# Performance work log

Measured on AMD Instinct MI355X. Metric: run time of the kernel, lower is better.

## Reference

```python
import jax, jax.numpy as jnp
import numpy as np
from jax import lax

VOCAB = 50257; IN_DIM = 1024; MEM = 1024
ATT_UNITS = 256; HOPS = 16
H1 = 1024; H2 = 512; H3 = 256; CLASSES = 5
N = 512  # maxlen == number of tree nodes (pad() is a no-op, penalty mask is zero)


def _build_tree(n):
    # Binary heap tree relabeled to DFS post-order ranks, so children always
    # have smaller rank than their parent and H accumulates in the same order
    # as the original recursive torch code.
    order = []
    def post(j):
        for c in (2 * j + 1, 2 * j + 2):
            if c < n:
                post(c)
        order.append(j)
    post(0)
    rank = {j: r for r, j in enumerate(order)}
    child_idx = np.zeros((n, 2), np.int32)
    mask = np.zeros((n, 2), np.float32)
    for j in range(n):
        r = rank[j]
        for k, c in enumerate((2 * j + 1, 2 * j + 2)):
            if c < n:
                child_idx[r, k] = rank[c]
                mask[r, k] = 1.0
    return jnp.asarray(child_idx), jnp.asarray(mask)


def setup_inputs() -> dict:
    key = jax.random.key(0)
    ks = jax.random.split(key, 24)
    def w(k, shape, s=0.05):
        return jax.random.normal(k, shape, jnp.float32) * s
    child_idx, child_mask = _build_tree(N)
    return {
        "linputs": jax.random.randint(ks[0], (N,), 0, VOCAB, jnp.int32),
        "rinputs": jax.random.randint(ks[1], (N,), 0, VOCAB, jnp.int32),
        "child_idx": child_idx,
        "child_mask": child_mask,
        "emb": w(ks[2], (VOCAB, IN_DIM)),
        "w_ioux": w(ks[3], (3 * MEM, IN_DIM)), "b_ioux": w(ks[4], (3 * MEM,)),
        "w_iouh": w(ks[5], (3 * MEM, MEM)), "b_iouh": w(ks[6], (3 * MEM,)),
        "w_fx": w(ks[7], (MEM, IN_DIM)), "b_fx": w(ks[8], (MEM,)),
        "w_fh": w(ks[9], (MEM, MEM)), "b_fh": w(ks[10], (MEM,)),
        "ws1": w(ks[11], (ATT_UNITS, MEM)),
        "ws2": w(ks[12], (HOPS, ATT_UNITS)),
        "wf": w(ks[13], (1, MEM, H1)),
        "w_lat": w(ks[14], (1, HOPS)), "b_lat": w(ks[15], (1,)),
        "w_fc": w(ks[16], (H2, 3 * H1)), "b_fc": w(ks[17], (H2,)),
        "w_out": w(ks[18], (H3, H2)), "b_out": w(ks[19], (H3,)),
        "w_out1": w(ks[20], (CLASSES, H3)), "b_out1": w(ks[21], (CLASSES,)),
    }


def _tree_lstm(x, child_idx, child_mask, w_ioux, b_ioux, w_iouh, b_iouh,
               w_fx, b_fx, w_fh, b_fh):
    # x: [N, in_dim]; nodes in post-order (children before parent).
    # Leaf case of the original (single all-zero child) is reproduced exactly
    # by masked (zero) child rows: child_h_sum = 0 and sum(f * child_c) = 0.
    n = x.shape[0]
    mem = w_fh.shape[0]
    x_iou = x @ w_ioux.T + b_ioux  # [N, 3M], precomputed input projections
    x_f = x @ w_fx.T + b_fx        # [N, M]

    def step(carry, xs):
        C, Hs = carry
        i, ci, m, xiou, xf = xs
        ch = Hs[ci] * m[:, None]   # [2, M] masked child hidden states
        cc = C[ci] * m[:, None]    # [2, M] masked child cell states
        iou = xiou + ch.sum(0) @ w_iouh.T + b_iouh
        ig, og, ug = jnp.split(iou, 3)
        ig = jax.nn.sigmoid(ig); og = jax.nn.sigmoid(og); ug = jnp.tanh(ug)
        f = jax.nn.sigmoid(ch @ w_fh.T + b_fh + xf)  # [2, M] forget per child
        c = ig * ug + (f * cc).sum(0)
        h = og * jnp.tanh(c)
        return (C.at[i].set(c), Hs.at[i].set(h)), None

    z = jnp.zeros((n, mem), x.dtype)
    (C, Hs), _ = lax.scan(step, (z, z),
                          (jnp.arange(n), child_idx, child_mask, x_iou, x_f))
    return Hs  # H stacked in DFS post-order; root hidden is Hs[-1]


def _attend(H, ws1, ws2):
    # H: [N, M]; N == maxlen so the penalty term of the original is all-zero.
    hbar = jnp.tanh(H @ ws1.T)                           # [N, att_units]
    alphas = jax.nn.softmax((hbar @ ws2.T).T, axis=-1)   # [hops, N]
    return alphas @ H, alphas[None]                      # [hops, M], [1, hops, N]


def reference(linputs, rinputs, child_idx, child_mask, emb,
              w_ioux, b_ioux, w_iouh, b_iouh, w_fx, b_fx, w_fh, b_fh,
              ws1, ws2, wf, w_lat, b_lat, w_fc, b_fc, w_out, b_out,
              w_out1, b_out1):
    tl = lambda tok: _tree_lstm(emb[tok], child_idx, child_mask,
                                w_ioux, b_ioux, w_iouh, b_iouh,
                                w_fx, b_fx, w_fh, b_fh)
    Hl = tl(linputs)
    Hr = tl(rinputs)
    Ml, attl = _attend(Hl, ws1, ws2)
    Mr, attr = _attend(Hr, ws1, ws2)
    lstate = jax.nn.relu(Ml @ wf[0])   # [hops, H1]
    rstate = jax.nn.relu(Mr @ wf[0])
    # lat_att applied on transposed matrix == left-multiply by its weight row
    lvec = w_lat @ lstate + b_lat      # [1, H1]
    rvec = w_lat @ rstate + b_lat
    fr = jnp.concatenate([jnp.abs(lvec - rvec), lvec * rvec,
                          0.5 * (lvec + rvec)], axis=1)  # [1, 3*H1]
    fc = jax.nn.leaky_relu(fr @ w_fc.T + b_fc, 0.01)
    fc2 = jax.nn.sigmoid(fc @ w_out.T + b_out)
    out = jax.nn.log_softmax(fc2 @ w_out1.T + b_out1, axis=-1)  # [1, classes]
    return out, attl, attr
```

## Files before the change

kernel.cpp:

```cpp
#include <hip/hip_runtime.h>
#include <math.h>

#define NN 512
#define MEMD 1024

typedef __attribute__((ext_vector_type(8))) short short8;
typedef __attribute__((ext_vector_type(4))) float float4v;

struct Sched {
  int child0[NN]; int child1[NN];
  float m0[NN]; float m1[NN];
  int chrow[2 * NN];
  int order[NN];
  int lvl_off[12];
};

constexpr void post_order_rec(int j, int n, int (&ord)[NN], int& cnt) {
  if (2 * j + 1 < n) post_order_rec(2 * j + 1, n, ord, cnt);
  if (2 * j + 2 < n) post_order_rec(2 * j + 2, n, ord, cnt);
  ord[cnt++] = j;
}

constexpr Sched make_sched() {
  Sched s{};
  int ord[NN] = {}; int cnt = 0;
  post_order_rec(0, NN, ord, cnt);
  int rank[NN] = {};
  for (int r = 0; r < NN; ++r) rank[ord[r]] = r;
  for (int j = 0; j < NN; ++j) {
    int r = rank[j];
    int c0 = 2 * j + 1, c1 = 2 * j + 2;
    s.child0[r] = (c0 < NN) ? rank[c0] : 0;
    s.m0[r] = (c0 < NN) ? 1.0f : 0.0f;
    s.child1[r] = (c1 < NN) ? rank[c1] : 0;
    s.m1[r] = (c1 < NN) ? 1.0f : 0.0f;
  }
  int h[NN] = {};
  for (int r = 0; r < NN; ++r) {
    int hh = 0;
    if (s.m0[r] > 0.0f) { int t = h[s.child0[r]] + 1; if (t > hh) hh = t; }
    if (s.m1[r] > 0.0f) { int t = h[s.child1[r]] + 1; if (t > hh) hh = t; }
    h[r] = hh;
  }
  int counts[12] = {};
  for (int r = 0; r < NN; ++r) counts[h[r]]++;
  s.lvl_off[0] = 0;
  for (int l = 0; l < 11; ++l) s.lvl_off[l + 1] = s.lvl_off[l] + counts[l];
  int pos[12] = {};
  for (int l = 0; l < 12; ++l) pos[l] = s.lvl_off[l];
  for (int r = 0; r < NN; ++r) s.order[pos[h[r]]++] = r;
  for (int slot = 0; slot < NN; ++slot) {
    int r = s.order[slot];
    s.chrow[2 * slot + 0] = (s.m0[r] > 0.f) ? s.child0[r] : -1;
    s.chrow[2 * slot + 1] = (s.m1[r] > 0.f) ? s.child1[r] : -1;
  }
  return s;
}

static constexpr Sched g_sched = make_sched();
__constant__ Sched c_sched = g_sched;

__device__ __forceinline__ float sigm(float x) { return 1.0f / (1.0f + expf(-x)); }

__device__ __forceinline__ unsigned short f2bf(float f) {
  union { float f; unsigned int u; } v; v.f = f;
  unsigned int r = v.u + 0x7fffu + ((v.u >> 16) & 1u);
  return (unsigned short)(r >> 16);
}

__device__ __forceinline__ void glds16(const unsigned short* g, unsigned short* l) {
  __builtin_amdgcn_global_load_lds(
      (const __attribute__((address_space(1))) void*)g,
      (__attribute__((address_space(3))) void*)l, 16, 0, 0);
}

__global__ __launch_bounds__(256) void k_cast_w(
    const float* __restrict__ w_ioux, const float* __restrict__ w_fx,
    const float* __restrict__ w_iouh, const float* __restrict__ w_fh,
    const float* __restrict__ ws1,
    unsigned short* __restrict__ Wx, unsigned short* __restrict__ Wh,
    unsigned short* __restrict__ Ws1b)
{
  const int b = (int)blockIdx.x;
  const float* src; unsigned short* dst;
  if (b < 4096) {
    dst = Wx + (size_t)b * 1024;
    src = (b < 3072) ? w_ioux + (size_t)b * 1024 : w_fx + (size_t)(b - 3072) * 1024;
  } else if (b < 8192) {
    int r = b - 4096;
    dst = Wh + (size_t)r * 1024;
    src = (r < 3072) ? w_iouh + (size_t)r * 1024 : w_fh + (size_t)(r - 3072) * 1024;
  } else {
    int r = b - 8192;
    dst = Ws1b + (size_t)r * 1024;
    src = ws1 + (size_t)r * 1024;
  }
  const int t4 = threadIdx.x * 4;
  float4 v = *(const float4*)(src + t4);
  ushort4 o;
  o.x = f2bf(v.x); o.y = f2bf(v.y); o.z = f2bf(v.z); o.w = f2bf(v.w);
  *(ushort4*)(dst + t4) = o;
}

__global__ __launch_bounds__(256) void k_cast_emb(
    const int* __restrict__ lin, const int* __restrict__ rin,
    const float* __restrict__ emb, unsigned short* __restrict__ Ae,
    unsigned short* __restrict__ Hb)
{
  const int r = (int)blockIdx.x;
  if (r == 1024) {
    ushort4 z; z.x = 0; z.y = 0; z.z = 0; z.w = 0;
    *(ushort4*)(Hb + (size_t)1024 * 1024 + threadIdx.x * 4) = z;
    return;
  }
  const int tok = (r < 512) ? lin[r] : rin[r - 512];
  const float* src = emb + (size_t)tok * 1024;
  const int t4 = threadIdx.x * 4;
  float4 v = *(const float4*)(src + t4);
  ushort4 o;
  o.x = f2bf(v.x); o.y = f2bf(v.y); o.z = f2bf(v.z); o.w = f2bf(v.w);
  *(ushort4*)(Ae + (size_t)r * 1024 + t4) = o;
}

__global__ __launch_bounds__(256) void k_gemm(
    const unsigned short* __restrict__ A, const unsigned short* __restrict__ B,
    float* __restrict__ Cout, int M, int N, int off, int R)
{
  __shared__ unsigned short As[2][128 * 64];
  __shared__ unsigned short Bs[2][128 * 64];
  const int tid = threadIdx.x;
  const int L = tid & 63, w = tid >> 6;
  const int bx = (int)blockIdx.x, by = (int)blockIdx.y;
  const int z = (int)blockIdx.z;
  const int nt = 16 / (int)gridDim.z;
  const int k0 = z * nt * 64;
  const int q = (L & 7) ^ (L >> 3);

  const unsigned short* ga[4];
  const unsigned short* gb[4];
  #pragma unroll
  for (int i = 0; i < 4; ++i) {
    int c = w * 4 + i;
    int r = 8 * c + (L >> 3);
    int u = bx * 128 + r;
    int arow;
    if (off < 0) {
      arow = u;
    } else {
      if (u >= 4 * R) arow = 1024;
      else {
        int t = (u >= 2 * R) ? 1 : 0;
        int rr = u - t * 2 * R;
        int ch = c_sched.chrow[2 * (off + (rr >> 1)) + (rr & 1)];
        arow = (ch < 0) ? 1024 : t * 512 + ch;
      }
    }
    ga[i] = A + (size_t)arow * 1024 + k0 + q * 8;
    gb[i] = B + (size_t)(by * 128 + r) * 1024 + k0 + q * 8;
  }

  float4v acc[4][4];
  #pragma unroll
  for (int i = 0; i < 4; ++i)
    #pragma unroll
    for (int j = 0; j < 4; ++j) acc[i][j] = (float4v)(0.0f);

  const int wm = (w & 1) * 64, wn = (w >> 1) * 64;
  const int lr = L & 15, lq = L >> 4;

  #pragma unroll
  for (int i = 0; i < 4; ++i) {
    glds16(ga[i], &As[0][(w * 4 + i) * 512]);
    glds16(gb[i], &Bs[0][(w * 4 + i) * 512]);
    ga[i] += 64; gb[i] += 64;
  }
  __syncthreads();

  int cur = 0;
  for (int kk = 0; kk < nt; ++kk) {
    if (kk + 1 < nt) {
      #pragma unroll
      for (int i = 0; i < 4; ++i) {
        glds16(ga[i], &As[cur ^ 1][(w * 4 + i) * 512]);
        glds16(gb[i], &Bs[cur ^ 1][(w * 4 + i) * 512]);
        ga[i] += 64; gb[i] += 64;
      }
    }
    const unsigned short* Ac = &As[cur][0];
    const unsigned short* Bc = &Bs[cur][0];
    #pragma unroll
    for (int kh = 0; kh < 2; ++kh) {
      short8 af[4], bf[4];
      #pragma unroll
      for (int mi = 0; mi < 4; ++mi) {
        int tr = wm + mi * 16 + lr;
        af[mi] = *(const short8*)(Ac + tr * 64 + (((kh * 4 + lq) ^ (tr & 7)) * 8));
      }
      #pragma unroll
      for (int ni = 0; ni < 4; ++ni) {
        int tr = wn + ni * 16 + lr;
        bf[ni] = *(const short8*)(Bc + tr * 64 + (((kh * 4 + lq) ^ (tr & 7)) * 8));
      }
      #pragma unroll
      for (int mi = 0; mi < 4; ++mi)
        #pragma unroll
        for (int ni = 0; ni < 4; ++ni)
          acc[mi][ni] = __builtin_amdgcn_mfma_f32_16x16x32_bf16(
              af[mi], bf[ni], acc[mi][ni], 0, 0, 0);
    }
    __syncthreads();
    cur ^= 1;
  }

  float* Cz = Cout + (size_t)z * M * N;
  #pragma unroll
  for (int mi = 0; mi < 4; ++mi) {
    #pragma unroll
    for (int reg = 0; reg < 4; ++reg) {
      int gr = bx * 128 + wm + mi * 16 + lq * 4 + reg;
      if (gr < M) {
        #pragma unroll
        for (int ni = 0; ni < 4; ++ni) {
          int gc = by * 128 + wn + ni * 16 + lr;
          Cout[(size_t)z * M * N + (size_t)gr * N + gc] = acc[mi][ni][reg];
        }
      }
    }
  }
  (void)Cz;
}

__global__ __launch_bounds__(256) void k_cell_leaf(
    const float* __restrict__ XO,
    const float* __restrict__ b_ioux, const float* __restrict__ b_iouh,
    float* __restrict__ H, float* __restrict__ C, unsigned short* __restrict__ Hb)
{
  const int s = (int)blockIdx.x;
  const int t = s >> 8, idx = s & 255;
  const int node = c_sched.order[idx];
  const size_t row = (size_t)t * 512 + node;
  for (int d = threadIdx.x; d < MEMD; d += 256) {
    float gi = XO[row * 4096 + d] + b_ioux[d] + b_iouh[d];
    float go = XO[row * 4096 + 1024 + d] + b_ioux[1024 + d] + b_iouh[1024 + d];
    float gu = XO[row * 4096 + 2048 + d] + b_ioux[2048 + d] + b_iouh[2048 + d];
    float cv = sigm(gi) * tanhf(gu);
    float hv = sigm(go) * tanhf(cv);
    C[row * MEMD + d] = cv;
    H[row * MEMD + d] = hv;
    Hb[row * MEMD + d] = f2bf(hv);
  }
}

__global__ __launch_bounds__(256) void k_cell_nl(
    const float* __restrict__ XO, const float* __restrict__ LO,
    const float* __restrict__ b_ioux, const float* __restrict__ b_iouh,
    const float* __restrict__ b_fx, const float* __restrict__ b_fh,
    float* __restrict__ H, float* __restrict__ C, unsigned short* __restrict__ Hb,
    int off, int R, int kz)
{
  const int s = (int)blockIdx.x;
  const int t = s / R, idx = s % R;
  const int node = c_sched.order[off + idx];
  const int c0 = c_sched.child0[node], c1 = c_sched.child1[node];
  const float m0 = c_sched.m0[node], m1 = c_sched.m1[node];
  const size_t row = (size_t)t * 512 + node;
  const size_t u0 = (size_t)(2 * s) * 4096;
  const size_t u1 = (size_t)(2 * s + 1) * 4096;
  const size_t lslab = (size_t)(4 * R) * 4096;
  for (int d = threadIdx.x; d < MEMD; d += 256) {
    float l_i = 0.f, l_o = 0.f, l_u = 0.f, l_f0 = 0.f, l_f1 = 0.f;
    for (int zz = 0; zz < kz; ++zz) {
      const float* Lz = LO + (size_t)zz * lslab;
      l_i  += Lz[u0 + d]        + Lz[u1 + d];
      l_o  += Lz[u0 + 1024 + d] + Lz[u1 + 1024 + d];
      l_u  += Lz[u0 + 2048 + d] + Lz[u1 + 2048 + d];
      l_f0 += Lz[u0 + 3072 + d];
      l_f1 += Lz[u1 + 3072 + d];
    }
    float gi = XO[row * 4096 + d] + l_i + b_ioux[d] + b_iouh[d];
    float go = XO[row * 4096 + 1024 + d] + l_o + b_ioux[1024 + d] + b_iouh[1024 + d];
    float gu = XO[row * 4096 + 2048 + d] + l_u + b_ioux[2048 + d] + b_iouh[2048 + d];
    float xf = XO[row * 4096 + 3072 + d] + b_fx[d] + b_fh[d];
    float f0 = sigm(l_f0 + xf);
    float f1 = sigm(l_f1 + xf);
    float cc0 = m0 * C[((size_t)t * 512 + c0) * MEMD + d];
    float cc1 = m1 * C[((size_t)t * 512 + c1) * MEMD + d];
    float cv = sigm(gi) * tanhf(gu) + f0 * cc0 + f1 * cc1;
    float hv = sigm(go) * tanhf(cv);
    C[row * MEMD + d] = cv;
    H[row * MEMD + d] = hv;
    Hb[row * MEMD + d] = f2bf(hv);
  }
}

__global__ __launch_bounds__(256) void k_logits(
    const float* __restrict__ HBR, const float* __restrict__ ws2,
    float* __restrict__ logits)
{
  __shared__ float hb[128][65];
  __shared__ float w2[16][256];
  const int b = (int)blockIdx.x;
  const int t = b / 4;
  const int n0 = (b % 4) * 128;
  const int tid = threadIdx.x;
  for (int e2 = tid; e2 < 16 * 256; e2 += 256) w2[e2 / 256][e2 % 256] = ws2[e2];
  const int n = tid & 127;
  const int hbase = (tid >> 7) * 8;
  float acc[8] = {};
  for (int a0 = 0; a0 < 256; a0 += 64) {
    __syncthreads();
    for (int e2 = tid; e2 < 128 * 64; e2 += 256) {
      int rr = e2 >> 6, aa = e2 & 63;
      size_t idx = (size_t)(t * 512 + n0 + rr) * 256 + a0 + aa;
      float v = HBR[idx] + HBR[262144 + idx] + HBR[2 * 262144 + idx]
              + HBR[3 * 262144 + idx];
      hb[rr][aa] = tanhf(v);
    }
    __syncthreads();
    for (int aa = 0; aa < 64; ++aa) {
      float v = hb[n][aa];
      #pragma unroll
      for (int hh = 0; hh < 8; ++hh) acc[hh] += v * w2[hbase + hh][a0 + aa];
    }
  }
  #pragma unroll
  for (int hh = 0; hh < 8; ++hh)
    logits[(size_t)(t * 16 + hbase + hh) * 512 + n0 + n] = acc[hh];
}

__global__ __launch_bounds__(256) void k_attnM(
    const float* __restrict__ LG, const float* __restrict__ H,
    float* __restrict__ M, float* __restrict__ out)
{
  __shared__ float al[16][512];
  const int b = (int)blockIdx.x;
  const int t = b >> 2;
  const int m0 = (b & 3) * 256;
  const int tid = threadIdx.x;
  for (int e2 = tid; e2 < 16 * 512; e2 += 256)
    al[e2 >> 9][e2 & 511] = LG[(size_t)t * 8192 + e2];
  __syncthreads();
  const int h = tid >> 4, i = tid & 15;
  float mx = -1e30f;
  #pragma unroll
  for (int j = 0; j < 32; ++j) mx = fmaxf(mx, al[h][i + 16 * j]);
  #pragma unroll
  for (int m2 = 8; m2 >= 1; m2 >>= 1) mx = fmaxf(mx, __shfl_xor(mx, m2, 64));
  float ev[32]; float s = 0.f;
  #pragma unroll
  for (int j = 0; j < 32; ++j) { ev[j] = expf(al[h][i + 16 * j] - mx); s += ev[j]; }
  #pragma unroll
  for (int m2 = 8; m2 >= 1; m2 >>= 1) s += __shfl_xor(s, m2, 64);
  float inv = 1.0f / s;
  #pragma unroll
  for (int j = 0; j < 32; ++j) al[h][i + 16 * j] = ev[j] * inv;
  __syncthreads();
  if ((b & 3) == 0) {
    for (int e2 = tid; e2 < 8192; e2 += 256)
      out[5 + (size_t)t * 8192 + e2] = al[e2 >> 9][e2 & 511];
  }
  float acc[16] = {};
  for (int n = 0; n < 512; ++n) {
    float hv = H[((size_t)t * 512 + n) * MEMD + m0 + tid];
    #pragma unroll
    for (int hh = 0; hh < 16; ++hh) acc[hh] += al[hh][n] * hv;
  }
  #pragma unroll
  for (int hh = 0; hh < 16; ++hh)
    M[((size_t)t * 16 + hh) * MEMD + m0 + tid] = acc[hh];
}

__global__ __launch_bounds__(256) void k_lstate(
    const float* __restrict__ M, const float* __restrict__ wf,
    float* __restrict__ tmp)
{
  __shared__ float Ms[4][1024];
  const int b = (int)blockIdx.x;
  const int t = b / 16;
  const int rem = b % 16;
  const int h0 = (rem / 4) * 4;
  const int o0 = (rem % 4) * 256;
  const int tid = threadIdx.x;
  for (int e2 = tid; e2 < 4 * 1024; e2 += 256)
    Ms[e2 >> 10][e2 & 1023] = M[((size_t)t * 16 + h0 + (e2 >> 10)) * MEMD + (e2 & 1023)];
  __syncthreads();
  float acc[4] = {};
  for (int m = 0; m < 1024; ++m) {
    float wv = wf[(size_t)m * 1024 + o0 + tid];
    #pragma unroll
    for (int h = 0; h < 4; ++h) acc[h] += Ms[h][m] * wv;
  }
  #pragma unroll
  for (int h = 0; h < 4; ++h)
    tmp[((size_t)t * 16 + h0 + h) * 1024 + o0 + tid] = acc[h];
}

__global__ __launch_bounds__(256) void k_fr(
    const float* __restrict__ tmp,
    const float* __restrict__ w_lat, const float* __restrict__ b_lat,
    float* __restrict__ FR)
{
  __shared__ float wl[16];
  const int tid = threadIdx.x;
  if (tid < 16) wl[tid] = w_lat[tid];
  __syncthreads();
  const int o = blockIdx.x * 256 + tid;
  const float blat = b_lat[0];
  float lv = blat, rv = blat;
  #pragma unroll
  for (int h = 0; h < 16; ++h) {
    lv += wl[h] * fmaxf(tmp[(size_t)h * 1024 + o], 0.0f);
    rv += wl[h] * fmaxf(tmp[(size_t)(16 + h) * 1024 + o], 0.0f);
  }
  FR[o] = fabsf(lv - rv);
  FR[1024 + o] = lv * rv;
  FR[2048 + o] = 0.5f * (lv + rv);
}

__global__ __launch_bounds__(256) void k_fc(
    const float* __restrict__ FR, const float* __restrict__ w_fc,
    const float* __restrict__ b_fc, float* __restrict__ FC)
{
  const int j = (int)blockIdx.x;
  const int tid = threadIdx.x;
  const float* wrow = w_fc + (size_t)j * 3072;
  float acc = 0.f;
  #pragma unroll
  for (int i = 0; i < 12; ++i) {
    int k = tid + i * 256;
    acc += FR[k] * wrow[k];
  }
  __shared__ float red[256];
  red[tid] = acc;
  __syncthreads();
  for (int s2 = 128; s2 > 0; s2 >>= 1) {
    if (tid < s2) red[tid] += red[tid + s2];
    __syncthreads();
  }
  if (tid == 0) {
    float v = red[0] + b_fc[j];
    FC[j] = (v > 0.f) ? v : 0.01f * v;
  }
}

__global__ __launch_bounds__(256) void k_fc2final(
    const float* __restrict__ FC, const float* __restrict__ w_out,
    const float* __restrict__ b_out, const float* __restrict__ w_out1,
    const float* __restrict__ b_out1, float* __restrict__ out)
{
  __shared__ float sh[256];
  __shared__ float lg5[5];
  const int tid = threadIdx.x;
  const float* wrow = w_out + (size_t)tid * 512;
  float acc = 0.f;
  #pragma unroll 8
  for (int k = 0; k < 512; ++k) acc += FC[k] * wrow[k];
  sh[tid] = 1.0f / (1.0f + expf(-(acc + b_out[tid])));
  __syncthreads();
  if (tid < 160) {
    const int cls = tid >> 5, lane = tid & 31;
    float a = 0.f;
    #pragma unroll
    for (int j = 0; j < 8; ++j) {
      int k = lane + 32 * j;
      a += sh[k] * w_out1[(size_t)cls * 256 + k];
    }
    #pragma unroll
    for (int m2 = 16; m2 >= 1; m2 >>= 1) a += __shfl_xor(a, m2, 64);
    if (lane == 0) lg5[cls] = a + b_out1[cls];
  }
  __syncthreads();
  if (tid == 0) {
    float mx = lg5[0];
    for (int k = 1; k < 5; ++k) mx = fmaxf(mx, lg5[k]);
    float s2 = 0.f;
    for (int k = 0; k < 5; ++k) s2 += expf(lg5[k] - mx);
    float lse = mx + logf(s2);
    for (int k = 0; k < 5; ++k) out[k] = lg5[k] - lse;
  }
}

extern "C" void kernel_launch(void* const* d_in, const int* in_sizes, int n_in,
                              void* d_out, int out_size, void* d_ws, size_t ws_size,
                              hipStream_t stream)
{
  const int*   lin    = (const int*)d_in[0];
  const int*   rin    = (const int*)d_in[1];
  const float* emb    = (const float*)d_in[4];
  const float* w_ioux = (const float*)d_in[5];
  const float* b_ioux = (const float*)d_in[6];
  const float* w_iouh = (const float*)d_in[7];
  const float* b_iouh = (const float*)d_in[8];
  const float* w_fx   = (const float*)d_in[9];
  const float* b_fx   = (const float*)d_in[10];
  const float* w_fh   = (const float*)d_in[11];
  const float* b_fh   = (const float*)d_in[12];
  const float* ws1    = (const float*)d_in[13];
  const float* ws2    = (const float*)d_in[14];
  const float* wf     = (const float*)d_in[15];
  const float* w_lat  = (const float*)d_in[16];
  const float* b_lat  = (const float*)d_in[17];
  const float* w_fc   = (const float*)d_in[18];
  const float* b_fc   = (const float*)d_in[19];
  const float* w_out  = (const float*)d_in[20];
  const float* b_out  = (const float*)d_in[21];
  const float* w_out1 = (const float*)d_in[22];
  const float* b_out1 = (const float*)d_in[23];
  float* out = (float*)d_out;

  float* fws  = (float*)d_ws;
  float* XO   = fws;
  float* LO   = XO + 1024 * 4096;
  float* H    = LO + 1024 * 4096;
  float* C    = H + 1024 * 1024;
  float* HBR  = C + 1024 * 1024;
  float* LG   = HBR + 4 * 1024 * 256;
  float* MB   = LG + 16384;
  float* TMP  = MB + 32768;
  float* FR   = TMP + 32768;
  float* FC   = FR + 3072;
  unsigned short* Ae   = (unsigned short*)(FC + 512);
  unsigned short* Wx   = Ae + 1024 * 1024;
  unsigned short* Wh   = Wx + 4096 * 1024;
  unsigned short* Hb   = Wh + 4096 * 1024;
  unsigned short* Ws1b = Hb + 1025 * 1024;

  k_cast_w<<<8448, 256, 0, stream>>>(w_ioux, w_fx, w_iouh, w_fh, ws1, Wx, Wh, Ws1b);
  k_cast_emb<<<1025, 256, 0, stream>>>(lin, rin, emb, Ae, Hb);

  k_gemm<<<dim3(8, 32, 1), 256, 0, stream>>>(Ae, Wx, XO, 1024, 4096, -1, 0);

  k_cell_leaf<<<512, 256, 0, stream>>>(XO, b_ioux, b_iouh, H, C, Hb);

  for (int l = 1; l < 11; ++l) {
    int off = g_sched.lvl_off[l];
    int R = g_sched.lvl_off[l + 1] - off;
    if (R <= 0) continue;
    int M4 = 4 * R;
    int gx = (M4 + 127) / 128;
    int kz = (M4 <= 128) ? 4 : 2;
    k_gemm<<<dim3(gx, 32, kz), 256, 0, stream>>>(Hb, Wh, LO, M4, 4096, off, R);
    k_cell_nl<<<2 * R, 256, 0, stream>>>(XO, LO, b_ioux, b_iouh, b_fx, b_fh,
                                         H, C, Hb, off, R, kz);
  }

  k_gemm<<<dim3(8, 2, 4), 256, 0, stream>>>(Hb, Ws1b, HBR, 1024, 256, -1, 0);

  k_logits<<<8, 256, 0, stream>>>(HBR, ws2, LG);
  k_attnM<<<8, 256, 0, stream>>>(LG, H, MB, out);
  k_lstate<<<32, 256, 0, stream>>>(MB, wf, TMP);
  k_fr<<<4, 256, 0, stream>>>(TMP, w_lat, b_lat, FR);
  k_fc<<<512, 256, 0, stream>>>(FR, w_fc, b_fc, FC);
  k_fc2final<<<1, 256, 0, stream>>>(FC, w_out, b_out, w_out1, b_out1, out);
}
```

Before: 728.4 us.

## Fuse whole pipeline into one persistent cooperative kernel with grid barriers

```diff
diff --git a/kernel.cpp b/kernel.cpp
--- a/kernel.cpp
+++ b/kernel.cpp
@@ -3,6 +3,7 @@
 
 #define NN 512
 #define MEMD 1024
+#define NBLK 256
 
 typedef __attribute__((ext_vector_type(8))) short short8;
 typedef __attribute__((ext_vector_type(4))) float float4v;
@@ -74,66 +75,51 @@
       (__attribute__((address_space(3))) void*)l, 16, 0, 0);
 }
 
-__global__ __launch_bounds__(256) void k_cast_w(
-    const float* __restrict__ w_ioux, const float* __restrict__ w_fx,
-    const float* __restrict__ w_iouh, const float* __restrict__ w_fh,
-    const float* __restrict__ ws1,
-    unsigned short* __restrict__ Wx, unsigned short* __restrict__ Wh,
-    unsigned short* __restrict__ Ws1b)
+struct KArgs {
+  const int* lin; const int* rin;
+  const float* emb;
+  const float* w_ioux; const float* b_ioux;
+  const float* w_iouh; const float* b_iouh;
+  const float* w_fx; const float* b_fx;
+  const float* w_fh; const float* b_fh;
+  const float* ws1; const float* ws2; const float* wf;
+  const float* w_lat; const float* b_lat;
+  const float* w_fc; const float* b_fc;
+  const float* w_out; const float* b_out;
+  const float* w_out1; const float* b_out1;
+  float* out;
+  float* XO; float* H; float* C; float* HBR; float* LG; float* M; float* TMP;
+  float* FR; float* FC;
+  unsigned short* Ae; unsigned short* Wxp; unsigned short* Whp;
+  unsigned short* Hb; unsigned short* Ws1b;
+  unsigned int* sc; unsigned int* sg;
+};
+
+__device__ __forceinline__ void gsync(unsigned int* sc, unsigned int* sg) {
+  __syncthreads();
+  if (threadIdx.x == 0) {
+    unsigned int g = __hip_atomic_load(sg, __ATOMIC_RELAXED, __HIP_MEMORY_SCOPE_AGENT);
+    unsigned int a = __hip_atomic_fetch_add(sc, 1u, __ATOMIC_ACQ_REL, __HIP_MEMORY_SCOPE_AGENT);
+    if (a == (unsigned int)(NBLK - 1)) {
+      __hip_atomic_store(sc, 0u, __ATOMIC_RELAXED, __HIP_MEMORY_SCOPE_AGENT);
+      __hip_atomic_store(sg, g + 1u, __ATOMIC_RELEASE, __HIP_MEMORY_SCOPE_AGENT);
+    } else {
+      while (__hip_atomic_load(sg, __ATOMIC_RELAXED, __HIP_MEMORY_SCOPE_AGENT) == g)
+        __builtin_amdgcn_s_sleep(1);
+      (void)__hip_atomic_load(sg, __ATOMIC_ACQUIRE, __HIP_MEMORY_SCOPE_AGENT);
+    }
+  }
+  __syncthreads();
+}
+
+__device__ float* gemm_tile(
+    const unsigned short* __restrict__ A, const unsigned short* __restrict__ B,
+    int off, int R, int k0, int nt, int bx, int by, char* smem)
 {
-  const int b = (int)blockIdx.x;
-  const float* src; unsigned short* dst;
-  if (b < 4096) {
-    dst = Wx + (size_t)b * 1024;
-    src = (b < 3072) ? w_ioux + (size_t)b * 1024 : w_fx + (size_t)(b - 3072) * 1024;
-  } else if (b < 8192) {
-    int r = b - 4096;
-    dst = Wh + (size_t)r * 1024;
-    src = (r < 3072) ? w_iouh + (size_t)r * 1024 : w_fh + (size_t)(r - 3072) * 1024;
-  } else {
-    int r = b - 8192;
-    dst = Ws1b + (size_t)r * 1024;
-    src = ws1 + (size_t)r * 1024;
-  }
-  const int t4 = threadIdx.x * 4;
-  float4 v = *(const float4*)(src + t4);
-  ushort4 o;
-  o.x = f2bf(v.x); o.y = f2bf(v.y); o.z = f2bf(v.z); o.w = f2bf(v.w);
-  *(ushort4*)(dst + t4) = o;
-}
-
-__global__ __launch_bounds__(256) void k_cast_emb(
-    const int* __restrict__ lin, const int* __restrict__ rin,
-    const float* __restrict__ emb, unsigned short* __restrict__ Ae,
-    unsigned short* __restrict__ Hb)
-{
-  const int r = (int)blockIdx.x;
-  if (r == 1024) {
-    ushort4 z; z.x = 0; z.y = 0; z.z = 0; z.w = 0;
-    *(ushort4*)(Hb + (size_t)1024 * 1024 + threadIdx.x * 4) = z;
-    return;
-  }
-  const int tok = (r < 512) ? lin[r] : rin[r - 512];
-  const float* src = emb + (size_t)tok * 1024;
-  const int t4 = threadIdx.x * 4;
-  float4 v = *(const float4*)(src + t4);
-  ushort4 o;
-  o.x = f2bf(v.x); o.y = f2bf(v.y); o.z = f2bf(v.z); o.w = f2bf(v.w);
-  *(ushort4*)(Ae + (size_t)r * 1024 + t4) = o;
-}
-
-__global__ __launch_bounds__(256) void k_gemm(
-    const unsigned short* __restrict__ A, const unsigned short* __restrict__ B,
-    float* __restrict__ Cout, int M, int N, int off, int R)
-{
-  __shared__ unsigned short As[2][128 * 64];
-  __shared__ unsigned short Bs[2][128 * 64];
+  unsigned short* As = (unsigned short*)smem;
+  unsigned short* Bs = (unsigned short*)(smem + 32768);
   const int tid = threadIdx.x;
   const int L = tid & 63, w = tid >> 6;
-  const int bx = (int)blockIdx.x, by = (int)blockIdx.y;
-  const int z = (int)blockIdx.z;
-  const int nt = 16 / (int)gridDim.z;
-  const int k0 = z * nt * 64;
   const int q = (L & 7) ^ (L >> 3);
 
   const unsigned short* ga[4];
@@ -170,8 +156,8 @@
 
   #pragma unroll
   for (int i = 0; i < 4; ++i) {
-    glds16(ga[i], &As[0][(w * 4 + i) * 512]);
-    glds16(gb[i], &Bs[0][(w * 4 + i) * 512]);
+    glds16(ga[i], As + (w * 4 + i) * 512);
+    glds16(gb[i], Bs + (w * 4 + i) * 512);
     ga[i] += 64; gb[i] += 64;
   }
   __syncthreads();
@@ -181,13 +167,13 @@
     if (kk + 1 < nt) {
       #pragma unroll
       for (int i = 0; i < 4; ++i) {
-        glds16(ga[i], &As[cur ^ 1][(w * 4 + i) * 512]);
-        glds16(gb[i], &Bs[cur ^ 1][(w * 4 + i) * 512]);
+        glds16(ga[i], As + (cur ^ 1) * 8192 + (w * 4 + i) * 512);
+        glds16(gb[i], Bs + (cur ^ 1) * 8192 + (w * 4 + i) * 512);
         ga[i] += 64; gb[i] += 64;
       }
     }
-    const unsigned short* Ac = &As[cur][0];
-    const unsigned short* Bc = &Bs[cur][0];
+    const unsigned short* Ac = As + cur * 8192;
+    const unsigned short* Bc = Bs + cur * 8192;
     #pragma unroll
     for (int kh = 0; kh < 2; ++kh) {
       short8 af[4], bf[4];
@@ -212,271 +198,308 @@
     cur ^= 1;
   }
 
-  float* Cz = Cout + (size_t)z * M * N;
+  float* T = (float*)smem;
   #pragma unroll
-  for (int mi = 0; mi < 4; ++mi) {
+  for (int mi = 0; mi < 4; ++mi)
     #pragma unroll
     for (int reg = 0; reg < 4; ++reg) {
-      int gr = bx * 128 + wm + mi * 16 + lq * 4 + reg;
-      if (gr < M) {
+      int tr = wm + mi * 16 + lq * 4 + reg;
+      #pragma unroll
+      for (int ni = 0; ni < 4; ++ni)
+        T[tr * 128 + wn + ni * 16 + lr] = acc[mi][ni][reg];
+    }
+  __syncthreads();
+  return T;
+}
+
+__global__ __launch_bounds__(256) void k_mega(KArgs a)
+{
+  __shared__ __align__(16) char smem[65536];
+  const int bid = (int)blockIdx.x;
+  const int tid = (int)threadIdx.x;
+
+  {
+    const int t4 = tid * 4;
+    for (int u = bid; u < 9473; u += NBLK) {
+      if (u < 9472) {
+        const float* src; unsigned short* dst;
+        if (u < 4096) {
+          int r = u & 127, g = r >> 5;
+          int c = (u >> 7) * 32 + (r & 31);
+          src = (g < 3) ? a.w_ioux + (size_t)(g * 1024 + c) * 1024
+                        : a.w_fx + (size_t)c * 1024;
+          dst = a.Wxp + (size_t)u * 1024;
+        } else if (u < 8192) {
+          int p = u - 4096;
+          int r = p & 127, g = r >> 5;
+          int c = (p >> 7) * 32 + (r & 31);
+          src = (g < 3) ? a.w_iouh + (size_t)(g * 1024 + c) * 1024
+                        : a.w_fh + (size_t)c * 1024;
+          dst = a.Whp + (size_t)p * 1024;
+        } else if (u < 8448) {
+          int p = u - 8192;
+          src = a.ws1 + (size_t)p * 1024;
+          dst = a.Ws1b + (size_t)p * 1024;
+        } else {
+          int p = u - 8448;
+          int tok = (p < 512) ? a.lin[p] : a.rin[p - 512];
+          src = a.emb + (size_t)tok * 1024;
+          dst = a.Ae + (size_t)p * 1024;
+        }
+        float4 v = *(const float4*)(src + t4);
+        ushort4 o;
+        o.x = f2bf(v.x); o.y = f2bf(v.y); o.z = f2bf(v.z); o.w = f2bf(v.w);
+        *(ushort4*)(dst + t4) = o;
+      } else {
+        ushort4 z; z.x = 0; z.y = 0; z.z = 0; z.w = 0;
+        *(ushort4*)(a.Hb + (size_t)1024 * 1024 + t4) = z;
+      }
+    }
+  }
+  gsync(a.sc, a.sg);
+
+  {
+    int bx = bid >> 5, by = bid & 31;
+    float* T = gemm_tile(a.Ae, a.Wxp, -1, 0, 0, 16, bx, by, smem);
+    for (int e = tid; e < 128 * 128; e += 256) {
+      int rr = e >> 7, cc = e & 127, g = cc >> 5;
+      a.XO[(size_t)(bx * 128 + rr) * 4096 + g * 1024 + by * 32 + (cc & 31)] =
+          T[rr * 128 + cc];
+    }
+    for (int e = tid; e < 128 * 32; e += 256) {
+      int rr = e >> 5, ccl = e & 31;
+      int row = bx * 128 + rr;
+      int rank = row & 511;
+      if (c_sched.m0[rank] == 0.0f) {
+        int d = by * 32 + ccl;
+        float gi = T[rr * 128 + ccl]      + a.b_ioux[d]        + a.b_iouh[d];
+        float go = T[rr * 128 + 32 + ccl] + a.b_ioux[1024 + d] + a.b_iouh[1024 + d];
+        float gu = T[rr * 128 + 64 + ccl] + a.b_ioux[2048 + d] + a.b_iouh[2048 + d];
+        float cv = sigm(gi) * tanhf(gu);
+        float hv = sigm(go) * tanhf(cv);
+        a.C[(size_t)row * MEMD + d] = cv;
+        a.H[(size_t)row * MEMD + d] = hv;
+        a.Hb[(size_t)row * MEMD + d] = f2bf(hv);
+      }
+    }
+  }
+  gsync(a.sc, a.sg);
+
+  for (int l = 1; l <= 9; ++l) {
+    int off = c_sched.lvl_off[l];
+    int R = c_sched.lvl_off[l + 1] - off;
+    int gx = (4 * R + 127) >> 7;
+    int nb = gx << 5;
+    if (bid < nb) {
+      int bx = bid >> 5, by = bid & 31;
+      float* T = gemm_tile(a.Hb, a.Whp, off, R, 0, 16, bx, by, smem);
+      int rows = 4 * R - bx * 128; if (rows > 128) rows = 128;
+      int pairs = rows >> 1;
+      for (int e = tid; e < pairs * 32; e += 256) {
+        int p = e >> 5, ccl = e & 31;
+        int u0 = bx * 128 + 2 * p;
+        int tt = (u0 >= 2 * R) ? 1 : 0;
+        int rr = u0 - tt * 2 * R;
+        int slot = off + (rr >> 1);
+        int node = c_sched.order[slot];
+        int d = by * 32 + ccl;
+        size_t row = (size_t)tt * 512 + node;
+        const float* T0 = T + (2 * p) * 128;
+        const float* T1 = T + (2 * p + 1) * 128;
+        float gi = a.XO[row * 4096 + d]        + T0[ccl]      + T1[ccl]
+                 + a.b_ioux[d] + a.b_iouh[d];
+        float go = a.XO[row * 4096 + 1024 + d] + T0[32 + ccl] + T1[32 + ccl]
+                 + a.b_ioux[1024 + d] + a.b_iouh[1024 + d];
+        float gu = a.XO[row * 4096 + 2048 + d] + T0[64 + ccl] + T1[64 + ccl]
+                 + a.b_ioux[2048 + d] + a.b_iouh[2048 + d];
+        float xf = a.XO[row * 4096 + 3072 + d] + a.b_fx[d] + a.b_fh[d];
+        float f0 = sigm(T0[96 + ccl] + xf);
+        float f1 = sigm(T1[96 + ccl] + xf);
+        int c0 = c_sched.child0[node], c1 = c_sched.child1[node];
+        float cc0 = c_sched.m0[node] * a.C[((size_t)tt * 512 + c0) * MEMD + d];
+        float cc1 = c_sched.m1[node] * a.C[((size_t)tt * 512 + c1) * MEMD + d];
+        float cv = sigm(gi) * tanhf(gu) + f0 * cc0 + f1 * cc1;
+        float hv = sigm(go) * tanhf(cv);
+        a.C[row * MEMD + d] = cv;
+        a.H[row * MEMD + d] = hv;
+        a.Hb[row * MEMD + d] = f2bf(hv);
+      }
+    }
+    gsync(a.sc, a.sg);
+  }
+
+  if (bid < 64) {
+    int z = bid & 3, by = (bid >> 2) & 1, bx = bid >> 3;
+    float* T = gemm_tile(a.Hb, a.Ws1b, -1, 0, z * 256, 4, bx, by, smem);
+    for (int e = tid; e < 128 * 128; e += 256) {
+      int rr = e >> 7, cc = e & 127;
+      a.HBR[(size_t)z * 262144 + (size_t)(bx * 128 + rr) * 256 + by * 128 + cc] =
+          T[rr * 128 + cc];
+    }
+  }
+  gsync(a.sc, a.sg);
+
+  if (bid < 8) {
+    float* hb = (float*)smem;
+    float* w2 = (float*)(smem + 128 * 65 * 4);
+    const int t = bid >> 2;
+    const int n0 = (bid & 3) * 128;
+    for (int e = tid; e < 16 * 256; e += 256) w2[e] = a.ws2[e];
+    const int n = tid & 127;
+    const int hbase = (tid >> 7) * 8;
+    float acc2[8] = {};
+    for (int a0 = 0; a0 < 256; a0 += 64) {
+      __syncthreads();
+      for (int e = tid; e < 128 * 64; e += 256) {
+        int rr = e >> 6, aa = e & 63;
+        size_t idx = (size_t)(t * 512 + n0 + rr) * 256 + a0 + aa;
+        float v = a.HBR[idx] + a.HBR[262144 + idx] + a.HBR[2 * 262144 + idx]
+                + a.HBR[3 * 262144 + idx];
+        hb[rr * 65 + aa] = tanhf(v);
+      }
+      __syncthreads();
+      for (int aa = 0; aa < 64; ++aa) {
+        float v = hb[n * 65 + aa];
         #pragma unroll
-        for (int ni = 0; ni < 4; ++ni) {
-          int gc = by * 128 + wn + ni * 16 + lr;
-          Cout[(size_t)z * M * N + (size_t)gr * N + gc] = acc[mi][ni][reg];
-        }
-      }
-    }
-  }
-  (void)Cz;
-}
-
-__global__ __launch_bounds__(256) void k_cell_leaf(
-    const float* __restrict__ XO,
-    const float* __restrict__ b_ioux, const float* __restrict__ b_iouh,
-    float* __restrict__ H, float* __restrict__ C, unsigned short* __restrict__ Hb)
-{
-  const int s = (int)blockIdx.x;
-  const int t = s >> 8, idx = s & 255;
-  const int node = c_sched.order[idx];
-  const size_t row = (size_t)t * 512 + node;
-  for (int d = threadIdx.x; d < MEMD; d += 256) {
-    float gi = XO[row * 4096 + d] + b_ioux[d] + b_iouh[d];
-    float go = XO[row * 4096 + 1024 + d] + b_ioux[1024 + d] + b_iouh[1024 + d];
-    float gu = XO[row * 4096 + 2048 + d] + b_ioux[2048 + d] + b_iouh[2048 + d];
-    float cv = sigm(gi) * tanhf(gu);
-    float hv = sigm(go) * tanhf(cv);
-    C[row * MEMD + d] = cv;
-    H[row * MEMD + d] = hv;
-    Hb[row * MEMD + d] = f2bf(hv);
-  }
-}
-
-__global__ __launch_bounds__(256) void k_cell_nl(
-    const float* __restrict__ XO, const float* __restrict__ LO,
-    const float* __restrict__ b_ioux, const float* __restrict__ b_iouh,
-    const float* __restrict__ b_fx, const float* __restrict__ b_fh,
-    float* __restrict__ H, float* __restrict__ C, unsigned short* __restrict__ Hb,
-    int off, int R, int kz)
-{
-  const int s = (int)blockIdx.x;
-  const int t = s / R, idx = s % R;
-  const int node = c_sched.order[off + idx];
-  const int c0 = c_sched.child0[node], c1 = c_sched.child1[node];
-  const float m0 = c_sched.m0[node], m1 = c_sched.m1[node];
-  const size_t row = (size_t)t * 512 + node;
-  const size_t u0 = (size_t)(2 * s) * 4096;
-  const size_t u1 = (size_t)(2 * s + 1) * 4096;
-  const size_t lslab = (size_t)(4 * R) * 4096;
-  for (int d = threadIdx.x; d < MEMD; d += 256) {
-    float l_i = 0.f, l_o = 0.f, l_u = 0.f, l_f0 = 0.f, l_f1 = 0.f;
-    for (int zz = 0; zz < kz; ++zz) {
-      const float* Lz = LO + (size_t)zz * lslab;
-      l_i  += Lz[u0 + d]        + Lz[u1 + d];
-      l_o  += Lz[u0 + 1024 + d] + Lz[u1 + 1024 + d];
-      l_u  += Lz[u0 + 2048 + d] + Lz[u1 + 2048 + d];
-      l_f0 += Lz[u0 + 3072 + d];
-      l_f1 += Lz[u1 + 3072 + d];
-    }
-    float gi = XO[row * 4096 + d] + l_i + b_ioux[d] + b_iouh[d];
-    float go = XO[row * 4096 + 1024 + d] + l_o + b_ioux[1024 + d] + b_iouh[1024 + d];
-    float gu = XO[row * 4096 + 2048 + d] + l_u + b_ioux[2048 + d] + b_iouh[2048 + d];
-    float xf = XO[row * 4096 + 3072 + d] + b_fx[d] + b_fh[d];
-    float f0 = sigm(l_f0 + xf);
-    float f1 = sigm(l_f1 + xf);
-    float cc0 = m0 * C[((size_t)t * 512 + c0) * MEMD + d];
-    float cc1 = m1 * C[((size_t)t * 512 + c1) * MEMD + d];
-    float cv = sigm(gi) * tanhf(gu) + f0 * cc0 + f1 * cc1;
-    float hv = sigm(go) * tanhf(cv);
-    C[row * MEMD + d] = cv;
-    H[row * MEMD + d] = hv;
-    Hb[row * MEMD + d] = f2bf(hv);
-  }
-}
-
-__global__ __launch_bounds__(256) void k_logits(
-    const float* __restrict__ HBR, const float* __restrict__ ws2,
-    float* __restrict__ logits)
-{
-  __shared__ float hb[128][65];
-  __shared__ float w2[16][256];
-  const int b = (int)blockIdx.x;
-  const int t = b / 4;
-  const int n0 = (b % 4) * 128;
-  const int tid = threadIdx.x;
-  for (int e2 = tid; e2 < 16 * 256; e2 += 256) w2[e2 / 256][e2 % 256] = ws2[e2];
-  const int n = tid & 127;
-  const int hbase = (tid >> 7) * 8;
-  float acc[8] = {};
-  for (int a0 = 0; a0 < 256; a0 += 64) {
+        for (int hh = 0; hh < 8; ++hh) acc2[hh] += v * w2[(hbase + hh) * 256 + a0 + aa];
+      }
+    }
+    #pragma unroll
+    for (int hh = 0; hh < 8; ++hh)
+      a.LG[(size_t)(t * 16 + hbase + hh) * 512 + n0 + n] = acc2[hh];
+  }
+  gsync(a.sc, a.sg);
+
+  if (bid < 8) {
+    float* al = (float*)smem;
+    const int t = bid >> 2;
+    const int m0 = (bid & 3) * 256;
+    for (int e = tid; e < 8192; e += 256) al[e] = a.LG[(size_t)t * 8192 + e];
     __syncthreads();
-    for (int e2 = tid; e2 < 128 * 64; e2 += 256) {
-      int rr = e2 >> 6, aa = e2 & 63;
-      size_t idx = (size_t)(t * 512 + n0 + rr) * 256 + a0 + aa;
-      float v = HBR[idx] + HBR[262144 + idx] + HBR[2 * 262144 + idx]
-              + HBR[3 * 262144 + idx];
-      hb[rr][aa] = tanhf(v);
-    }
+    const int h = tid >> 4, i = tid & 15;
+    float mx = -1e30f;
+    #pragma unroll
+    for (int j = 0; j < 32; ++j) mx = fmaxf(mx, al[h * 512 + i + 16 * j]);
+    #pragma unroll
+    for (int m2 = 8; m2 >= 1; m2 >>= 1) mx = fmaxf(mx, __shfl_xor(mx, m2, 64));
+    float ev[32]; float s = 0.f;
+    #pragma unroll
+    for (int j = 0; j < 32; ++j) { ev[j] = expf(al[h * 512 + i + 16 * j] - mx); s += ev[j]; }
+    #pragma unroll
+    for (int m2 = 8; m2 >= 1; m2 >>= 1) s += __shfl_xor(s, m2, 64);
+    float inv = 1.0f / s;
+    #pragma unroll
+    for (int j = 0; j < 32; ++j) al[h * 512 + i + 16 * j] = ev[j] * inv;
     __syncthreads();
-    for (int aa = 0; aa < 64; ++aa) {
-      float v = hb[n][aa];
-      #pragma unroll
-      for (int hh = 0; hh < 8; ++hh) acc[hh] += v * w2[hbase + hh][a0 + aa];
-    }
-  }
-  #pragma unroll
-  for (int hh = 0; hh < 8; ++hh)
-    logits[(size_t)(t * 16 + hbase + hh) * 512 + n0 + n] = acc[hh];
-}
-
-__global__ __launch_bounds__(256) void k_attnM(
-    const float* __restrict__ LG, const float* __restrict__ H,
-    float* __restrict__ M, float* __restrict__ out)
-{
-  __shared__ float al[16][512];
-  const int b = (int)blockIdx.x;
-  const int t = b >> 2;
-  const int m0 = (b & 3) * 256;
-  const int tid = threadIdx.x;
-  for (int e2 = tid; e2 < 16 * 512; e2 += 256)
-    al[e2 >> 9][e2 & 511] = LG[(size_t)t * 8192 + e2];
-  __syncthreads();
-  const int h = tid >> 4, i = tid & 15;
-  float mx = -1e30f;
-  #pragma unroll
-  for (int j = 0; j < 32; ++j) mx = fmaxf(mx, al[h][i + 16 * j]);
-  #pragma unroll
-  for (int m2 = 8; m2 >= 1; m2 >>= 1) mx = fmaxf(mx, __shfl_xor(mx, m2, 64));
-  float ev[32]; float s = 0.f;
-  #pragma unroll
-  for (int j = 0; j < 32; ++j) { ev[j] = expf(al[h][i + 16 * j] - mx); s += ev[j]; }
-  #pragma unroll
-  for (int m2 = 8; m2 >= 1; m2 >>= 1) s += __shfl_xor(s, m2, 64);
-  float inv = 1.0f / s;
-  #pragma unroll
-  for (int j = 0; j < 32; ++j) al[h][i + 16 * j] = ev[j] * inv;
-  __syncthreads();
-  if ((b & 3) == 0) {
-    for (int e2 = tid; e2 < 8192; e2 += 256)
-      out[5 + (size_t)t * 8192 + e2] = al[e2 >> 9][e2 & 511];
-  }
-  float acc[16] = {};
-  for (int n = 0; n < 512; ++n) {
-    float hv = H[((size_t)t * 512 + n) * MEMD + m0 + tid];
-    #pragma unroll
-    for (int hh = 0; hh < 16; ++hh) acc[hh] += al[hh][n] * hv;
-  }
-  #pragma unroll
-  for (int hh = 0; hh < 16; ++hh)
-    M[((size_t)t * 16 + hh) * MEMD + m0 + tid] = acc[hh];
-}
-
-__global__ __launch_bounds__(256) void k_lstate(
-    const float* __restrict__ M, const float* __restrict__ wf,
-    float* __restrict__ tmp)
-{
-  __shared__ float Ms[4][1024];
-  const int b = (int)blockIdx.x;
-  const int t = b / 16;
-  const int rem = b % 16;
-  const int h0 = (rem / 4) * 4;
-  const int o0 = (rem % 4) * 256;
-  const int tid = threadIdx.x;
-  for (int e2 = tid; e2 < 4 * 1024; e2 += 256)
-    Ms[e2 >> 10][e2 & 1023] = M[((size_t)t * 16 + h0 + (e2 >> 10)) * MEMD + (e2 & 1023)];
-  __syncthreads();
-  float acc[4] = {};
-  for (int m = 0; m < 1024; ++m) {
-    float wv = wf[(size_t)m * 1024 + o0 + tid];
-    #pragma unroll
-    for (int h = 0; h < 4; ++h) acc[h] += Ms[h][m] * wv;
-  }
-  #pragma unroll
-  for (int h = 0; h < 4; ++h)
-    tmp[((size_t)t * 16 + h0 + h) * 1024 + o0 + tid] = acc[h];
-}
-
-__global__ __launch_bounds__(256) void k_fr(
-    const float* __restrict__ tmp,
-    const float* __restrict__ w_lat, const float* __restrict__ b_lat,
-    float* __restrict__ FR)
-{
-  __shared__ float wl[16];
-  const int tid = threadIdx.x;
-  if (tid < 16) wl[tid] = w_lat[tid];
-  __syncthreads();
-  const int o = blockIdx.x * 256 + tid;
-  const float blat = b_lat[0];
-  float lv = blat, rv = blat;
-  #pragma unroll
-  for (int h = 0; h < 16; ++h) {
-    lv += wl[h] * fmaxf(tmp[(size_t)h * 1024 + o], 0.0f);
-    rv += wl[h] * fmaxf(tmp[(size_t)(16 + h) * 1024 + o], 0.0f);
-  }
-  FR[o] = fabsf(lv - rv);
-  FR[1024 + o] = lv * rv;
-  FR[2048 + o] = 0.5f * (lv + rv);
-}
-
-__global__ __launch_bounds__(256) void k_fc(
-    const float* __restrict__ FR, const float* __restrict__ w_fc,
-    const float* __restrict__ b_fc, float* __restrict__ FC)
-{
-  const int j = (int)blockIdx.x;
-  const int tid = threadIdx.x;
-  const float* wrow = w_fc + (size_t)j * 3072;
-  float acc = 0.f;
-  #pragma unroll
-  for (int i = 0; i < 12; ++i) {
-    int k = tid + i * 256;
-    acc += FR[k] * wrow[k];
-  }
-  __shared__ float red[256];
-  red[tid] = acc;
-  __syncthreads();
-  for (int s2 = 128; s2 > 0; s2 >>= 1) {
-    if (tid < s2) red[tid] += red[tid + s2];
+    if ((bid & 3) == 0) {
+      for (int e = tid; e < 8192; e += 256)
+        a.out[5 + (size_t)t * 8192 + e] = al[e];
+    }
+    float acc3[16] = {};
+    for (int n = 0; n < 512; ++n) {
+      float hv = a.H[((size_t)t * 512 + n) * MEMD + m0 + tid];
+      #pragma unroll
+      for (int hh = 0; hh < 16; ++hh) acc3[hh] += al[hh * 512 + n] * hv;
+    }
+    #pragma unroll
+    for (int hh = 0; hh < 16; ++hh)
+      a.M[((size_t)t * 16 + hh) * MEMD + m0 + tid] = acc3[hh];
+  }
+  gsync(a.sc, a.sg);
+
+  if (bid < 32) {
+    float* Ms = (float*)smem;
+    const int t = bid / 16;
+    const int rem = bid % 16;
+    const int h0 = (rem / 4) * 4;
+    const int o0 = (rem % 4) * 256;
+    for (int e = tid; e < 4 * 1024; e += 256)
+      Ms[e] = a.M[((size_t)t * 16 + h0 + (e >> 10)) * MEMD + (e & 1023)];
     __syncthreads();
-  }
-  if (tid == 0) {
-    float v = red[0] + b_fc[j];
-    FC[j] = (v > 0.f) ? v : 0.01f * v;
-  }
-}
-
-__global__ __launch_bounds__(256) void k_fc2final(
-    const float* __restrict__ FC, const float* __restrict__ w_out,
-    const float* __restrict__ b_out, const float* __restrict__ w_out1,
-    const float* __restrict__ b_out1, float* __restrict__ out)
-{
-  __shared__ float sh[256];
-  __shared__ float lg5[5];
-  const int tid = threadIdx.x;
-  const float* wrow = w_out + (size_t)tid * 512;
-  float acc = 0.f;
-  #pragma unroll 8
-  for (int k = 0; k < 512; ++k) acc += FC[k] * wrow[k];
-  sh[tid] = 1.0f / (1.0f + expf(-(acc + b_out[tid])));
-  __syncthreads();
-  if (tid < 160) {
-    const int cls = tid >> 5, lane = tid & 31;
-    float a = 0.f;
-    #pragma unroll
-    for (int j = 0; j < 8; ++j) {
-      int k = lane + 32 * j;
-      a += sh[k] * w_out1[(size_t)cls * 256 + k];
-    }
-    #pragma unroll
-    for (int m2 = 16; m2 >= 1; m2 >>= 1) a += __shfl_xor(a, m2, 64);
-    if (lane == 0) lg5[cls] = a + b_out1[cls];
-  }
-  __syncthreads();
-  if (tid == 0) {
-    float mx = lg5[0];
-    for (int k = 1; k < 5; ++k) mx = fmaxf(mx, lg5[k]);
-    float s2 = 0.f;
-    for (int k = 0; k < 5; ++k) s2 += expf(lg5[k] - mx);
-    float lse = mx + logf(s2);
-    for (int k = 0; k < 5; ++k) out[k] = lg5[k] - lse;
+    float acc4[4] = {};
+    for (int m = 0; m < 1024; ++m) {
+      float wv = a.wf[(size_t)m * 1024 + o0 + tid];
+      #pragma unroll
+      for (int h = 0; h < 4; ++h) acc4[h] += Ms[h * 1024 + m] * wv;
+    }
+    #pragma unroll
+    for (int h = 0; h < 4; ++h)
+      a.TMP[((size_t)t * 16 + h0 + h) * 1024 + o0 + tid] = acc4[h];
+  }
+  gsync(a.sc, a.sg);
+
+  if (bid < 4) {
+    const int o = bid * 256 + tid;
+    const float blat = a.b_lat[0];
+    float lv = blat, rv = blat;
+    #pragma unroll
+    for (int h = 0; h < 16; ++h) {
+      float wlh = a.w_lat[h];
+      lv += wlh * fmaxf(a.TMP[(size_t)h * 1024 + o], 0.0f);
+      rv += wlh * fmaxf(a.TMP[(size_t)(16 + h) * 1024 + o], 0.0f);
+    }
+    a.FR[o] = fabsf(lv - rv);
+    a.FR[1024 + o] = lv * rv;
+    a.FR[2048 + o] = 0.5f * (lv + rv);
+  }
+  gsync(a.sc, a.sg);
+
+  {
+    float* red = (float*)smem;
+    for (int rep = 0; rep < 2; ++rep) {
+      int j = bid + rep * 256;
+      const float* wrow = a.w_fc + (size_t)j * 3072;
+      float acc5 = 0.f;
+      #pragma unroll
+      for (int i2 = 0; i2 < 12; ++i2) {
+        int k = tid + i2 * 256;
+        acc5 += a.FR[k] * wrow[k];
+      }
+      red[tid] = acc5;
+      __syncthreads();
+      for (int s2 = 128; s2 > 0; s2 >>= 1) {
+        if (tid < s2) red[tid] += red[tid + s2];
+        __syncthreads();
+      }
+      if (tid == 0) {
+        float v = red[0] + a.b_fc[j];
+        a.FC[j] = (v > 0.f) ? v : 0.01f * v;
+      }
+      __syncthreads();
+    }
+  }
+  gsync(a.sc, a.sg);
+
+  if (bid == 0) {
+    float* sh = (float*)smem;
+    float* lg5 = sh + 256;
+    const float* wrow = a.w_out + (size_t)tid * 512;
+    float acc6 = 0.f;
+    #pragma unroll 8
+    for (int k = 0; k < 512; ++k) acc6 += a.FC[k] * wrow[k];
+    sh[tid] = 1.0f / (1.0f + expf(-(acc6 + a.b_out[tid])));
+    __syncthreads();
+    if (tid < 160) {
+      const int cls = tid >> 5, lane = tid & 31;
+      float v = 0.f;
+      #pragma unroll
+      for (int j = 0; j < 8; ++j) {
+        int k = lane + 32 * j;
+        v += sh[k] * a.w_out1[(size_t)cls * 256 + k];
+      }
+      #pragma unroll
+      for (int m2 = 16; m2 >= 1; m2 >>= 1) v += __shfl_xor(v, m2, 64);
+      if (lane == 0) lg5[cls] = v + a.b_out1[cls];
+    }
+    __syncthreads();
+    if (tid == 0) {
+      float mx = lg5[0];
+      for (int k = 1; k < 5; ++k) mx = fmaxf(mx, lg5[k]);
+      float s2 = 0.f;
+      for (int k = 0; k < 5; ++k) s2 += expf(lg5[k] - mx);
+      float lse = mx + logf(s2);
+      for (int k = 0; k < 5; ++k) a.out[k] = lg5[k] - lse;
+    }
   }
 }
 
@@ -484,72 +507,51 @@
                               void* d_out, int out_size, void* d_ws, size_t ws_size,
                               hipStream_t stream)
 {
-  const int*   lin    = (const int*)d_in[0];
-  const int*   rin    = (const int*)d_in[1];
-  const float* emb    = (const float*)d_in[4];
-  const float* w_ioux = (const float*)d_in[5];
-  const float* b_ioux = (const float*)d_in[6];
-  const float* w_iouh = (const float*)d_in[7];
-  const float* b_iouh = (const float*)d_in[8];
-  const float* w_fx   = (const float*)d_in[9];
-  const float* b_fx   = (const float*)d_in[10];
-  const float* w_fh   = (const float*)d_in[11];
-  const float* b_fh   = (const float*)d_in[12];
-  const float* ws1    = (const float*)d_in[13];
-  const float* ws2    = (const float*)d_in[14];
-  const float* wf     = (const float*)d_in[15];
-  const float* w_lat  = (const float*)d_in[16];
-  const float* b_lat  = (const float*)d_in[17];
-  const float* w_fc   = (const float*)d_in[18];
-  const float* b_fc   = (const float*)d_in[19];
-  const float* w_out  = (const float*)d_in[20];
-  const float* b_out  = (const float*)d_in[21];
-  const float* w_out1 = (const float*)d_in[22];
-  const float* b_out1 = (const float*)d_in[23];
-  float* out = (float*)d_out;
-
-  float* fws  = (float*)d_ws;
-  float* XO   = fws;
-  float* LO   = XO + 1024 * 4096;
-  float* H    = LO + 1024 * 4096;
-  float* C    = H + 1024 * 1024;
-  float* HBR  = C + 1024 * 1024;
-  float* LG   = HBR + 4 * 1024 * 256;
-  float* MB   = LG + 16384;
-  float* TMP  = MB + 32768;
-  float* FR   = TMP + 32768;
-  float* FC   = FR + 3072;
-  unsigned short* Ae   = (unsigned short*)(FC + 512);
-  unsigned short* Wx   = Ae + 1024 * 1024;
-  unsigned short* Wh   = Wx + 4096 * 1024;
-  unsigned short* Hb   = Wh + 4096 * 1024;
-  unsigned short* Ws1b = Hb + 1025 * 1024;
-
-  k_cast_w<<<8448, 256, 0, stream>>>(w_ioux, w_fx, w_iouh, w_fh, ws1, Wx, Wh, Ws1b);
-  k_cast_emb<<<1025, 256, 0, stream>>>(lin, rin, emb, Ae, Hb);
-
-  k_gemm<<<dim3(8, 32, 1), 256, 0, stream>>>(Ae, Wx, XO, 1024, 4096, -1, 0);
-
-  k_cell_leaf<<<512, 256, 0, stream>>>(XO, b_ioux, b_iouh, H, C, Hb);
-
-  for (int l = 1; l < 11; ++l) {
-    int off = g_sched.lvl_off[l];
-    int R = g_sched.lvl_off[l + 1] - off;
-    if (R <= 0) continue;
-    int M4 = 4 * R;
-    int gx = (M4 + 127) / 128;
-    int kz = (M4 <= 128) ? 4 : 2;
-    k_gemm<<<dim3(gx, 32, kz), 256, 0, stream>>>(Hb, Wh, LO, M4, 4096, off, R);
-    k_cell_nl<<<2 * R, 256, 0, stream>>>(XO, LO, b_ioux, b_iouh, b_fx, b_fh,
-                                         H, C, Hb, off, R, kz);
-  }
-
-  k_gemm<<<dim3(8, 2, 4), 256, 0, stream>>>(Hb, Ws1b, HBR, 1024, 256, -1, 0);
-
-  k_logits<<<8, 256, 0, stream>>>(HBR, ws2, LG);
-  k_attnM<<<8, 256, 0, stream>>>(LG, H, MB, out);
-  k_lstate<<<32, 256, 0, stream>>>(MB, wf, TMP);
-  k_fr<<<4, 256, 0, stream>>>(TMP, w_lat, b_lat, FR);
-  k_fc<<<512, 256, 0, stream>>>(FR, w_fc, b_fc, FC);
-  k_fc2final<<<1, 256, 0, stream>>>(FC, w_out, b_out, w_out1, b_out1, out);
-}
+  KArgs ka;
+  ka.lin    = (const int*)d_in[0];
+  ka.rin    = (const int*)d_in[1];
+  ka.emb    = (const float*)d_in[4];
+  ka.w_ioux = (const float*)d_in[5];
+  ka.b_ioux = (const float*)d_in[6];
+  ka.w_iouh = (const float*)d_in[7];
+  ka.b_iouh = (const float*)d_in[8];
+  ka.w_fx   = (const float*)d_in[9];
+  ka.b_fx   = (const float*)d_in[10];
+  ka.w_fh   = (const float*)d_in[11];
+  ka.b_fh   = (const float*)d_in[12];
+  ka.ws1    = (const float*)d_in[13];
+  ka.ws2    = (const float*)d_in[14];
+  ka.wf     = (const float*)d_in[15];
+  ka.w_lat  = (const float*)d_in[16];
+  ka.b_lat  = (const float*)d_in[17];
+  ka.w_fc   = (const float*)d_in[18];
+  ka.b_fc   = (const float*)d_in[19];
+  ka.w_out  = (const float*)d_in[20];
+  ka.b_out  = (const float*)d_in[21];
+  ka.w_out1 = (const float*)d_in[22];
+  ka.b_out1 = (const float*)d_in[23];
+  ka.out    = (float*)d_out;
+
+  float* fws = (float*)d_ws;
+  ka.XO  = fws;
+  ka.H   = ka.XO  + 1024 * 4096;
+  ka.C   = ka.H   + 1024 * 1024;
+  ka.HBR = ka.C   + 1024 * 1024;
+  ka.LG  = ka.HBR + 4 * 1024 * 256;
+  ka.M   = ka.LG  + 16384;
+  ka.TMP = ka.M   + 32768;
+  ka.FR  = ka.TMP + 32768;
+  ka.FC  = ka.FR  + 3072;
+  ka.Ae   = (unsigned short*)(ka.FC + 512);
+  ka.Wxp  = ka.Ae  + 1024 * 1024;
+  ka.Whp  = ka.Wxp + 4096 * 1024;
+  ka.Hb   = ka.Whp + 4096 * 1024;
+  ka.Ws1b = ka.Hb  + 1025 * 1024;
+  ka.sc   = (unsigned int*)(ka.Ws1b + 256 * 1024);
+  ka.sg   = ka.sc + 64;
+
+  hipMemsetAsync((void*)ka.sc, 0, 512, stream);
+  void* params[1] = { (void*)&ka };
+  hipLaunchCooperativeKernel((const void*)k_mega, dim3(NBLK), dim3(256),
+                             params, 0, stream);
+}
```

Result: slower. 877.3 us (+20.4%).
